# Kernel optimization log

Measured on AMD Instinct MI355X. Metric: run time of the kernel, lower is better.

Reference implementation:

```python
import jax, jax.numpy as jnp
import numpy as np


def setup_inputs() -> dict:
    key = jax.random.key(0)
    ks = jax.random.split(key, 8)
    B, C, W, H = 16, 256, 48, 48
    d = C // 8
    return {
        "x": jax.random.normal(ks[0], (B, C, W, H), dtype=jnp.float32),
        "Wq": jax.random.normal(ks[1], (d, C), dtype=jnp.float32) * 0.05,
        "bq": jax.random.normal(ks[2], (d,), dtype=jnp.float32) * 0.05,
        "Wk": jax.random.normal(ks[3], (d, C), dtype=jnp.float32) * 0.05,
        "bk": jax.random.normal(ks[4], (d,), dtype=jnp.float32) * 0.05,
        "Wv": jax.random.normal(ks[5], (C, C), dtype=jnp.float32) * 0.05,
        "bv": jax.random.normal(ks[6], (C,), dtype=jnp.float32) * 0.05,
        "gamma": jax.random.normal(ks[7], (1,), dtype=jnp.float32),
    }


def reference(x, Wq, bq, Wk, bk, Wv, bv, gamma):
    B, C, W, H = x.shape
    N = W * H
    xf = x.reshape(B, C, N)  # [B, C, N]
    # 1x1 convs == per-pixel linear projections
    q = jnp.einsum('dc,bcn->bdn', Wq, xf) + bq[None, :, None]  # [B, d, N]
    k = jnp.einsum('dc,bcn->bdn', Wk, xf) + bk[None, :, None]  # [B, d, N]
    v = jnp.einsum('oc,bcn->bon', Wv, xf) + bv[None, :, None]  # [B, C, N]
    # energy[b, i, j] = <q[:, i], k[:, j]>  (i = query pixel, j = key pixel)
    energy = jnp.einsum('bdi,bdj->bij', q, k)  # [B, N, N]
    # NOTE: softmax over dim=1 (the QUERY axis), faithful to nn.Softmax(dim=1)
    attention = jax.nn.softmax(energy, axis=1)
    # out[b, c, i] = sum_j v[b, c, j] * attention[b, i, j]
    out = jnp.einsum('bcj,bij->bci', v, attention)
    out = out.reshape(B, C, W, H)
    return gamma * out + x
```

## Files before the change

kernel.cpp:

```cpp
#include <hip/hip_runtime.h>

#define Bx 16
#define Cx 256
#define Dx 32
#define Nx 2304

typedef _Float16 f16;
typedef _Float16 f16x4 __attribute__((ext_vector_type(4)));
typedef _Float16 f16x8 __attribute__((ext_vector_type(8)));
typedef float    f32x4 __attribute__((ext_vector_type(4)));
typedef float    f32x16 __attribute__((ext_vector_type(16)));
typedef unsigned int u32x2 __attribute__((ext_vector_type(2)));
typedef unsigned int u32x4 __attribute__((ext_vector_type(4)));

#define MFMA_K16(a, b, c) __builtin_amdgcn_mfma_f32_32x32x16_f16((a), (b), (c), 0, 0, 0)
#define EXP2F(x) __builtin_amdgcn_exp2f(x)

__device__ __forceinline__ f16x8 swap_pack(f16x4 a, f16x4 b) {
    u32x2 au = __builtin_bit_cast(u32x2, a);
    u32x2 bu = __builtin_bit_cast(u32x2, b);
    unsigned a0 = au[0], a1 = au[1], b0 = bu[0], b1 = bu[1];
    asm("v_permlane32_swap_b32 %0, %1" : "+v"(a0), "+v"(b0));
    asm("v_permlane32_swap_b32 %0, %1" : "+v"(a1), "+v"(b1));
    u32x4 r = {a0, a1, b0, b1};
    return __builtin_bit_cast(f16x8, r);
}

__global__ __launch_bounds__(256) void wall_prep(
    const float* __restrict__ Wq, const float* __restrict__ bq,
    const float* __restrict__ Wk, const float* __restrict__ bk,
    const float* __restrict__ Wv, const float* __restrict__ bv,
    f16* __restrict__ Wall, float* __restrict__ bias_all) {
    int r = blockIdx.x;
    int t = threadIdx.x;
    const float SC = 1.4426950408889634f;
    const float* src;
    float scale, bsc;
    if (r < 32)      { src = Wq + (size_t)r * Cx;        scale = SC;  bsc = bq[r] * SC; }
    else if (r < 64) { src = Wk + (size_t)(r - 32) * Cx; scale = 1.f; bsc = bk[r - 32]; }
    else             { src = Wv + (size_t)(r - 64) * Cx; scale = 1.f; bsc = bv[r - 64]; }
    Wall[(size_t)r * Cx + t] = (f16)(src[t] * scale);
    if (t == 0) bias_all[r] = bsc;
}

#define PG_ROWLEN 24
__global__ __launch_bounds__(256) void proj_gemm(
    const float* __restrict__ x,
    const f16* __restrict__ Wall, const float* __restrict__ bias_all,
    f16* __restrict__ qws, f16* __restrict__ kws, f16* __restrict__ vws) {
    __shared__ __align__(16) f16 xs[256 * PG_ROWLEN];
    int bid = blockIdx.x;
    int nt = bid % 9;   bid /= 9;
    int rt = bid % 10;  bid /= 10;
    int b  = bid;
    int n0 = nt * 256;
    int r0 = rt * 32;
    int t  = threadIdx.x;
    int wv = t >> 6, il = t & 31, h = (t >> 5) & 1;

    const float* xb = x + (size_t)b * Cx * Nx + n0 + t;
    const f16*   wp = Wall + (size_t)(r0 + il) * Cx + h * 8;

    f32x16 acc[2];
    acc[0] = (f32x16){};
    acc[1] = (f32x16){};
    int nb = wv * 64 + il;

    for (int ks = 0; ks < 16; ++ks) {
        float xv[16];
#pragma unroll
        for (int kk = 0; kk < 16; ++kk)
            xv[kk] = xb[(size_t)(ks * 16 + kk) * Nx];
        f16x8 p0, p1;
#pragma unroll
        for (int kk = 0; kk < 8; ++kk) {
            p0[kk] = (f16)xv[kk];
            p1[kk] = (f16)xv[8 + kk];
        }
        __syncthreads();
        *(f16x8*)&xs[t * PG_ROWLEN]     = p0;
        *(f16x8*)&xs[t * PG_ROWLEN + 8] = p1;
        __syncthreads();

        f16x8 wf  = *(const f16x8*)(wp + ks * 16);
        f16x8 xf0 = *(const f16x8*)&xs[nb * PG_ROWLEN + h * 8];
        f16x8 xf1 = *(const f16x8*)&xs[(nb + 32) * PG_ROWLEN + h * 8];
        __builtin_amdgcn_s_setprio(1);
        if (rt < 2) {
            acc[0] = MFMA_K16(wf, xf0, acc[0]);
            acc[1] = MFMA_K16(wf, xf1, acc[1]);
        } else {
            acc[0] = MFMA_K16(xf0, wf, acc[0]);
            acc[1] = MFMA_K16(xf1, wf, acc[1]);
        }
        __builtin_amdgcn_s_setprio(0);
    }

    if (rt < 2) {
        f16* dst = rt ? kws : qws;
#pragma unroll
        for (int f = 0; f < 2; ++f) {
            int n = n0 + wv * 64 + f * 32 + il;
            size_t base = ((size_t)b * Nx + n) * Dx + 4 * h;
#pragma unroll
            for (int g = 0; g < 4; ++g) {
                f16x4 o;
#pragma unroll
                for (int rr = 0; rr < 4; ++rr)
                    o[rr] = (f16)(acc[f][4 * g + rr] +
                                  bias_all[r0 + 8 * g + 4 * h + rr]);
                *(f16x4*)(dst + base + 8 * g) = o;
            }
        }
    } else {
        int c = (rt - 2) * 32 + il;
        float bvv = bias_all[r0 + il];
#pragma unroll
        for (int f = 0; f < 2; ++f) {
            size_t base = ((size_t)b * Cx + c) * Nx + n0 + wv * 64 + f * 32 + 4 * h;
#pragma unroll
            for (int g = 0; g < 4; ++g) {
                f16x4 o;
#pragma unroll
                for (int rr = 0; rr < 4; ++rr)
                    o[rr] = (f16)(acc[f][4 * g + rr] + bvv);
                *(f16x4*)(vws + base + 8 * g) = o;
            }
        }
    }
}

__global__ __launch_bounds__(256, 4) void col_stats(
    const f16* __restrict__ qhi, const f16* __restrict__ khi,
    float* __restrict__ s) {
    __shared__ float part[4][32];
    int jt = blockIdx.x % 72;
    int b  = blockIdx.x / 72;
    int j0 = jt * 32;
    int t  = threadIdx.x;
    int w  = t >> 6;
    int il = t & 31, h = (t >> 5) & 1;

    f16x8 kh[2];
#pragma unroll
    for (int ks = 0; ks < 2; ++ks)
        kh[ks] = *(const f16x8*)(khi + ((size_t)b * Nx + j0 + il) * Dx + h * 8 + ks * 16);

    f32x16 sacc = {};
    for (int it = w * 18; it < w * 18 + 18; ++it) {
        f16x8 qh[2];
#pragma unroll
        for (int ks = 0; ks < 2; ++ks)
            qh[ks] = *(const f16x8*)(qhi + ((size_t)b * Nx + it * 32 + il) * Dx + h * 8 + ks * 16);
        f32x16 e = {};
        __builtin_amdgcn_s_setprio(1);
        e = MFMA_K16(kh[0], qh[0], e);
        e = MFMA_K16(kh[1], qh[1], e);
        __builtin_amdgcn_s_setprio(0);
#pragma unroll
        for (int r = 0; r < 16; ++r) sacc[r] += EXP2F(e[r]);
    }
#pragma unroll
    for (int r = 0; r < 16; ++r) {
        float v = sacc[r];
        for (int msk = 1; msk <= 16; msk <<= 1) v += __shfl_xor(v, msk);
        if (il == 0) part[w][(r & 3) + 8 * (r >> 2) + 4 * h] = v;
    }
    __syncthreads();
    if (t < 32)
        s[(size_t)b * Nx + j0 + t] =
            part[0][t] + part[1][t] + part[2][t] + part[3][t];
}

__global__ __launch_bounds__(128, 3) void attn_out(
    const f16* __restrict__ qhi, const f16* __restrict__ khi,
    const f16* __restrict__ vhi,
    const float* __restrict__ s, const float* __restrict__ x,
    const float* __restrict__ gamma, float* __restrict__ out) {
    __shared__ __align__(16) float rs[Nx];
    __shared__ float red[64][33];
    int blk = blockIdx.x;
    int w4   = blk & 3;  blk >>= 2;
    int it64 = blk % 36;
    int b    = blk / 36;
    int i0   = it64 * 64;
    int c0   = w4 * 64;
    int t = threadIdx.x;
    int jh   = t >> 6;
    int lane = t & 63;
    int il = t & 31, h = (t >> 5) & 1;

    {
        const f32x4* s4 = (const f32x4*)(s + (size_t)b * Nx);
        f32x4* rs4 = (f32x4*)rs;
        for (int r = t; r < Nx / 4; r += 128) {
            f32x4 v = s4[r];
            rs4[r] = (f32x4){1.0f / v[0], 1.0f / v[1], 1.0f / v[2], 1.0f / v[3]};
        }
    }
    __syncthreads();

    f16x8 qh[2][2];
#pragma unroll
    for (int itile = 0; itile < 2; ++itile)
#pragma unroll
        for (int ks = 0; ks < 2; ++ks)
            qh[itile][ks] = *(const f16x8*)(qhi +
                ((size_t)b * Nx + i0 + itile * 32 + il) * Dx + h * 8 + ks * 16);

    f32x16 acc[2][2];
#pragma unroll
    for (int a = 0; a < 2; ++a)
#pragma unroll
        for (int cgi = 0; cgi < 2; ++cgi) acc[a][cgi] = (f32x16){};

    int jb = jh * 36 * 32;
    const f16* kph = khi + ((size_t)b * Nx + jb + il) * Dx + h * 8;
    const f16* vph = vhi + ((size_t)b * Cx + c0 + il) * Nx + jb + h * 8;

    f16x8 kb[2][2];
    f16x8 vb[2][2][2];

#pragma unroll
    for (int ks = 0; ks < 2; ++ks) {
        kb[0][ks] = *(const f16x8*)(kph + ks * 16);
        kb[1][ks] = *(const f16x8*)(kph + 1024 + ks * 16);
    }
#pragma unroll
    for (int cg = 0; cg < 2; ++cg)
#pragma unroll
        for (int gp = 0; gp < 2; ++gp) {
            size_t voff = (size_t)cg * 32 * Nx + gp * 16;
            vb[0][cg][gp] = *(const f16x8*)(vph + voff);
            vb[1][cg][gp] = *(const f16x8*)(vph + voff + 32);
        }

#pragma unroll 2
    for (int jt = 0; jt < 36; ++jt) {
        int cur = jt & 1;
        int j0  = jb + jt * 32;
#pragma unroll
        for (int itile = 0; itile < 2; ++itile) {
            f32x16 e = {};
            __builtin_amdgcn_s_setprio(1);
            e = MFMA_K16(kb[cur][0], qh[itile][0], e);
            e = MFMA_K16(kb[cur][1], qh[itile][1], e);
            __builtin_amdgcn_s_setprio(0);
            f16x4 ph4[4];
#pragma unroll
            for (int g = 0; g < 4; ++g) {
                f32x4 rsv = *(const f32x4*)&rs[j0 + 8 * g + 4 * h];
#pragma unroll
                for (int jj = 0; jj < 4; ++jj)
                    ph4[g][jj] = (f16)(EXP2F(e[4 * g + jj]) * rsv[jj]);
            }
            f16x8 phK[2];
            phK[0] = swap_pack(ph4[0], ph4[1]);
            phK[1] = swap_pack(ph4[2], ph4[3]);
            __builtin_amdgcn_s_setprio(1);
#pragma unroll
            for (int cg = 0; cg < 2; ++cg)
#pragma unroll
                for (int gp = 0; gp < 2; ++gp)
                    acc[itile][cg] = MFMA_K16(vb[cur][cg][gp], phK[gp], acc[itile][cg]);
            __builtin_amdgcn_s_setprio(0);
        }
        int kn = (jt + 2 < 36) ? (jt + 2) * 1024 : 0;
#pragma unroll
        for (int ks = 0; ks < 2; ++ks)
            kb[cur][ks] = *(const f16x8*)(kph + kn + ks * 16);
        int vn = (jt + 2 < 36) ? (jt + 2) * 32 : 0;
#pragma unroll
        for (int cg = 0; cg < 2; ++cg)
#pragma unroll
            for (int gp = 0; gp < 2; ++gp) {
                size_t voff = (size_t)cg * 32 * Nx + vn + gp * 16;
                vb[cur][cg][gp] = *(const f16x8*)(vph + voff);
            }
    }

    float gm = gamma[0];
#pragma unroll
    for (int itile = 0; itile < 2; ++itile) {
        __syncthreads();
        if (jh == 1) {
#pragma unroll
            for (int cg = 0; cg < 2; ++cg)
#pragma unroll
                for (int r = 0; r < 16; ++r)
                    red[lane][cg * 16 + r] = acc[itile][cg][r];
        }
        __syncthreads();
        if (jh == 0) {
#pragma unroll
            for (int cg = 0; cg < 2; ++cg)
#pragma unroll
                for (int r = 0; r < 16; ++r) {
                    int c = c0 + cg * 32 + (r & 3) + 8 * (r >> 2) + 4 * h;
                    int i = i0 + itile * 32 + il;
                    size_t idx = ((size_t)b * Cx + c) * Nx + i;
                    out[idx] = x[idx] +
                        gm * (acc[itile][cg][r] + red[lane][cg * 16 + r]);
                }
        }
    }
}

extern "C" void kernel_launch(void* const* d_in, const int* in_sizes, int n_in,
                              void* d_out, int out_size, void* d_ws, size_t ws_size,
                              hipStream_t stream) {
    const float* x     = (const float*)d_in[0];
    const float* Wq    = (const float*)d_in[1];
    const float* bq    = (const float*)d_in[2];
    const float* Wk    = (const float*)d_in[3];
    const float* bk    = (const float*)d_in[4];
    const float* Wv    = (const float*)d_in[5];
    const float* bv    = (const float*)d_in[6];
    const float* gamma = (const float*)d_in[7];
    float* out = (float*)d_out;

    const size_t QK = (size_t)Bx * Nx * Dx;
    const size_t VN = (size_t)Bx * Cx * Nx;
    f16* qws = (f16*)d_ws;
    f16* kws = qws + QK;
    f16* vws = kws + QK;
    float* s = (float*)(vws + VN);
    f16* Wall = (f16*)(s + (size_t)Bx * Nx);
    float* bias_all = (float*)(Wall + 320 * Cx);

    wall_prep<<<320,            256, 0, stream>>>(Wq, bq, Wk, bk, Wv, bv, Wall, bias_all);
    proj_gemm<<<Bx * 10 * 9,    256, 0, stream>>>(x, Wall, bias_all, qws, kws, vws);
    col_stats<<<Bx * 72,        256, 0, stream>>>(qws, kws, s);
    attn_out <<<Bx * 36 * 4,    128, 0, stream>>>(qws, kws, vws, s, x, gamma, out);
}
```

Baseline: 278.9 us.

## Fold softmax normalizer into MFMA accumulator init, pack with cvt_pkrtz, swizzle XCDs

```diff
diff --git a/kernel.cpp b/kernel.cpp
--- a/kernel.cpp
+++ b/kernel.cpp
@@ -15,15 +15,19 @@
 
 #define MFMA_K16(a, b, c) __builtin_amdgcn_mfma_f32_32x32x16_f16((a), (b), (c), 0, 0, 0)
 #define EXP2F(x) __builtin_amdgcn_exp2f(x)
-
-__device__ __forceinline__ f16x8 swap_pack(f16x4 a, f16x4 b) {
-    u32x2 au = __builtin_bit_cast(u32x2, a);
-    u32x2 bu = __builtin_bit_cast(u32x2, b);
-    unsigned a0 = au[0], a1 = au[1], b0 = bu[0], b1 = bu[1];
+#define PKRTZ_U32(lo, hi) __builtin_bit_cast(unsigned, __builtin_amdgcn_cvt_pkrtz((lo), (hi)))
+
+__device__ __forceinline__ f16x8 swap_pack4(unsigned a0, unsigned a1,
+                                            unsigned b0, unsigned b1) {
     asm("v_permlane32_swap_b32 %0, %1" : "+v"(a0), "+v"(b0));
     asm("v_permlane32_swap_b32 %0, %1" : "+v"(a1), "+v"(b1));
     u32x4 r = {a0, a1, b0, b1};
     return __builtin_bit_cast(f16x8, r);
+}
+
+__device__ __forceinline__ int xcd_swz(int nwg8) {
+    int bid = blockIdx.x;
+    return (bid & 7) * nwg8 + (bid >> 3);
 }
 
 __global__ __launch_bounds__(256) void wall_prep(
@@ -49,7 +53,7 @@
     const f16* __restrict__ Wall, const float* __restrict__ bias_all,
     f16* __restrict__ qws, f16* __restrict__ kws, f16* __restrict__ vws) {
     __shared__ __align__(16) f16 xs[256 * PG_ROWLEN];
-    int bid = blockIdx.x;
+    int bid = xcd_swz(180);
     int nt = bid % 9;   bid /= 9;
     int rt = bid % 10;  bid /= 10;
     int b  = bid;
@@ -134,8 +138,9 @@
     const f16* __restrict__ qhi, const f16* __restrict__ khi,
     float* __restrict__ s) {
     __shared__ float part[4][32];
-    int jt = blockIdx.x % 72;
-    int b  = blockIdx.x / 72;
+    int blk = xcd_swz(144);
+    int jt = blk % 72;
+    int b  = blk / 72;
     int j0 = jt * 32;
     int t  = threadIdx.x;
     int w  = t >> 6;
@@ -179,7 +184,7 @@
     const float* __restrict__ gamma, float* __restrict__ out) {
     __shared__ __align__(16) float rs[Nx];
     __shared__ float red[64][33];
-    int blk = blockIdx.x;
+    int blk = xcd_swz(288);
     int w4   = blk & 3;  blk >>= 2;
     int it64 = blk % 36;
     int b    = blk / 36;
@@ -195,7 +200,8 @@
         f32x4* rs4 = (f32x4*)rs;
         for (int r = t; r < Nx / 4; r += 128) {
             f32x4 v = s4[r];
-            rs4[r] = (f32x4){1.0f / v[0], 1.0f / v[1], 1.0f / v[2], 1.0f / v[3]};
+            rs4[r] = (f32x4){-__log2f(v[0]), -__log2f(v[1]),
+                             -__log2f(v[2]), -__log2f(v[3])};
         }
     }
     __syncthreads();
@@ -239,24 +245,29 @@
     for (int jt = 0; jt < 36; ++jt) {
         int cur = jt & 1;
         int j0  = jb + jt * 32;
+        f32x16 ev;
+#pragma unroll
+        for (int g = 0; g < 4; ++g) {
+            f32x4 rv = *(const f32x4*)&rs[j0 + 8 * g + 4 * h];
+#pragma unroll
+            for (int jj = 0; jj < 4; ++jj) ev[4 * g + jj] = rv[jj];
+        }
 #pragma unroll
         for (int itile = 0; itile < 2; ++itile) {
-            f32x16 e = {};
+            f32x16 e;
             __builtin_amdgcn_s_setprio(1);
-            e = MFMA_K16(kb[cur][0], qh[itile][0], e);
+            e = MFMA_K16(kb[cur][0], qh[itile][0], ev);
             e = MFMA_K16(kb[cur][1], qh[itile][1], e);
             __builtin_amdgcn_s_setprio(0);
-            f16x4 ph4[4];
+            unsigned pk[4][2];
 #pragma unroll
             for (int g = 0; g < 4; ++g) {
-                f32x4 rsv = *(const f32x4*)&rs[j0 + 8 * g + 4 * h];
-#pragma unroll
-                for (int jj = 0; jj < 4; ++jj)
-                    ph4[g][jj] = (f16)(EXP2F(e[4 * g + jj]) * rsv[jj]);
+                pk[g][0] = PKRTZ_U32(EXP2F(e[4 * g]),     EXP2F(e[4 * g + 1]));
+                pk[g][1] = PKRTZ_U32(EXP2F(e[4 * g + 2]), EXP2F(e[4 * g + 3]));
             }
             f16x8 phK[2];
-            phK[0] = swap_pack(ph4[0], ph4[1]);
-            phK[1] = swap_pack(ph4[2], ph4[3]);
+            phK[0] = swap_pack4(pk[0][0], pk[0][1], pk[1][0], pk[1][1]);
+            phK[1] = swap_pack4(pk[2][0], pk[2][1], pk[3][0], pk[3][1]);
             __builtin_amdgcn_s_setprio(1);
 #pragma unroll
             for (int cg = 0; cg < 2; ++cg)
```

Result: faster. 259.6 us (-6.9%).
